# Optimization experiments

Measured on AMD Instinct MI355X. Metric: run time of the kernel, lower is better.

The kernel has to match this reference:

```python
import jax, jax.numpy as jnp
from jax import lax
import numpy as np

H, W = 4096, 4096
KH, KW = 15, 15


def setup_inputs() -> dict:
    key = jax.random.key(0)
    kx, kw = jax.random.split(key)
    X = jax.random.normal(kx, (H, W), dtype=jnp.float32)
    weight = jax.random.uniform(kw, (KH, KW), dtype=jnp.float32)
    bias = jnp.zeros((1,), dtype=jnp.float32)
    return {"X": X, "weight": weight, "bias": bias}


def reference(X, weight, bias):
    # Valid 2D cross-correlation (no kernel flip), matching corr2d.
    # lax.conv_general_dilated performs cross-correlation by default.
    out = lax.conv_general_dilated(
        X[None, None, :, :],            # NCHW: [1, 1, H, W]
        weight[None, None, :, :],       # OIHW: [1, 1, KH, KW]
        window_strides=(1, 1),
        padding="VALID",
    )
    return out[0, 0] + bias[0]          # [H-KH+1, W-KW+1]
```

## Files before the change

### kernel.cpp

```cpp
#include <hip/hip_runtime.h>
#include <hip/hip_bf16.h>

#define H_IN 4096
#define W_IN 4096
#define KH 15
#define KW 15
#define OH (H_IN - KH + 1)
#define OW (W_IN - KW + 1)

#define BM 64
#define BN 128
#define NJ (BN / 16)
#define SROWS (BM + KH - 1)
#define SCOLS 144
#define SSTR  152
#define SCH4 36
#define STAGE_N (SROWS * SCH4)
#define NLOAD 11

typedef __attribute__((ext_vector_type(8))) short short8;
typedef __attribute__((ext_vector_type(4))) float f32x4;

__device__ __forceinline__ ushort f2bf(float f) {
    __hip_bfloat16 h = __float2bfloat16(f);
    return __builtin_bit_cast(ushort, h);
}

__global__ __launch_bounds__(256)
void build_wfrags(const float* __restrict__ Wt, ushort* __restrict__ Bw)
{
    int idx = blockIdx.x * 256 + threadIdx.x;
    if (idx < KH * 64) {
        int kh = idx >> 6, l = idx & 63;
        int j = l & 15, k0 = (l >> 4) * 8;
        union { ushort u[8]; uint4 v; } t;
#pragma unroll
        for (int u = 0; u < 8; ++u) {
            int kw = k0 + u - j;
            t.u[u] = f2bf((kw >= 0 && kw < KW) ? Wt[kh * KW + kw] : 0.0f);
        }
        *reinterpret_cast<uint4*>(&Bw[idx * 8]) = t.v;
    }
}

__global__ __launch_bounds__(256, 4)
void conv2d_mfma_bf16(const float* __restrict__ X,
                      const ushort* __restrict__ Bw,
                      const float* __restrict__ Bias,
                      float* __restrict__ Out)
{
    __shared__ ushort s_x[SROWS * SSTR];

    const int tid = threadIdx.x;
    const int l = tid & 63;
    const int w = tid >> 6;
    const int ox0 = blockIdx.x * BN;
    const int oy0 = blockIdx.y * BM;
    const bool xint = (ox0 + SCOLS <= W_IN);

    float4 v[NLOAD];
#pragma unroll
    for (int k = 0; k < NLOAD; ++k) {
        int i = tid + 256 * k;
        if (i < STAGE_N) {
            int r  = i / SCH4;
            int c4 = i % SCH4;
            int gy = min(oy0 + r, H_IN - 1);
            const float* rp = X + (size_t)gy * W_IN;
            int gx = ox0 + c4 * 4;
            if (xint) {
                v[k] = *reinterpret_cast<const float4*>(rp + gx);
            } else {
                v[k].x = rp[min(gx + 0, W_IN - 1)];
                v[k].y = rp[min(gx + 1, W_IN - 1)];
                v[k].z = rp[min(gx + 2, W_IN - 1)];
                v[k].w = rp[min(gx + 3, W_IN - 1)];
            }
        }
    }
#pragma unroll
    for (int k = 0; k < NLOAD; ++k) {
        int i = tid + 256 * k;
        if (i < STAGE_N) {
            int r  = i / SCH4;
            int c4 = i % SCH4;
            uint2 pk;
            pk.x = (uint32_t)f2bf(v[k].x) | ((uint32_t)f2bf(v[k].y) << 16);
            pk.y = (uint32_t)f2bf(v[k].z) | ((uint32_t)f2bf(v[k].w) << 16);
            *reinterpret_cast<uint2*>(&s_x[r * SSTR + c4 * 4]) = pk;
        }
    }
    __syncthreads();

    const ushort* const bbase = Bw + l * 8;
    short8 bfr[KH];
#pragma unroll
    for (int kh = 0; kh < KH; ++kh)
        bfr[kh] = *reinterpret_cast<const short8*>(bbase + kh * 64 * 8);
    __builtin_amdgcn_sched_barrier(0);

    const ushort* const abase = &s_x[(w * 16 + (l & 15)) * SSTR + (l >> 4) * 8];

    f32x4 acc[NJ];
#pragma unroll
    for (int j = 0; j < NJ; ++j) acc[j] = (f32x4){0.f, 0.f, 0.f, 0.f};

#pragma unroll
    for (int kh = 0; kh < KH; ++kh) {
        const ushort* arow = abase + kh * SSTR;
#pragma unroll
        for (int j = 0; j < NJ; ++j) {
            short8 a = *reinterpret_cast<const short8*>(arow + j * 16);
            acc[j] = __builtin_amdgcn_mfma_f32_16x16x32_bf16(a, bfr[kh], acc[j], 0, 0, 0);
        }
    }

    const float b = Bias[0];
    const int orow0 = oy0 + w * 16 + (l >> 4) * 4;
    const int ocol  = ox0 + (l & 15);
    if (oy0 + BM <= OH && ox0 + BN <= OW) {
        float* op0 = &Out[(size_t)orow0 * OW + ocol];
#pragma unroll
        for (int j = 0; j < NJ; ++j) {
#pragma unroll
            for (int r = 0; r < 4; ++r)
                op0[(size_t)r * OW + j * 16] = acc[j][r] + b;
        }
    } else {
#pragma unroll
        for (int j = 0; j < NJ; ++j) {
            int oc = ocol + j * 16;
            if (oc < OW) {
#pragma unroll
                for (int r = 0; r < 4; ++r) {
                    int orow = orow0 + r;
                    if (orow < OH)
                        Out[(size_t)orow * OW + oc] = acc[j][r] + b;
                }
            }
        }
    }
}

extern "C" void kernel_launch(void* const* d_in, const int* in_sizes, int n_in,
                              void* d_out, int out_size, void* d_ws, size_t ws_size,
                              hipStream_t stream)
{
    const float* X    = (const float*)d_in[0];
    const float* Wt   = (const float*)d_in[1];
    const float* Bias = (const float*)d_in[2];
    float* Out        = (float*)d_out;
    ushort* Bw        = (ushort*)d_ws;

    hipLaunchKernelGGL(build_wfrags, dim3((KH * 64 + 255) / 256), dim3(256), 0, stream,
                       Wt, Bw);

    dim3 grid((OW + BN - 1) / BN,
              (OH + BM - 1) / BM);
    dim3 block(256);
    hipLaunchKernelGGL(conv2d_mfma_bf16, grid, block, 0, stream, X, Bw, Bias, Out);
}
```

Baseline: 43.62 us.

## Process two row tiles per block with register-prefetched next tile

Each block now handles two vertically adjacent output tiles. It issues the global loads for the next tile into registers before running the MFMA loop on the current one, then writes them to LDS between two barriers. Weight fragments are now loaded per kh inside the loop instead of being held in 15 registers up front, which lowers register pressure. The cost is half as many blocks, so less parallelism, plus extra barriers and weight reloads from global/L2 on every tile.

Result: slower. 48.44 us (+11.0%).

```diff
diff --git a/kernel.cpp b/kernel.cpp
--- a/kernel.cpp
+++ b/kernel.cpp
@@ -17,6 +17,7 @@
 #define SCH4 36
 #define STAGE_N (SROWS * SCH4)
 #define NLOAD 11
+#define TPB 2
 
 typedef __attribute__((ext_vector_type(8))) short short8;
 typedef __attribute__((ext_vector_type(4))) float f32x4;
@@ -43,22 +44,10 @@
     }
 }
 
-__global__ __launch_bounds__(256, 4)
-void conv2d_mfma_bf16(const float* __restrict__ X,
-                      const ushort* __restrict__ Bw,
-                      const float* __restrict__ Bias,
-                      float* __restrict__ Out)
+__device__ __forceinline__ void stage_issue(const float* __restrict__ X,
+                                            int oy0, int ox0, bool xint,
+                                            int tid, float4 (&v)[NLOAD])
 {
-    __shared__ ushort s_x[SROWS * SSTR];
-
-    const int tid = threadIdx.x;
-    const int l = tid & 63;
-    const int w = tid >> 6;
-    const int ox0 = blockIdx.x * BN;
-    const int oy0 = blockIdx.y * BM;
-    const bool xint = (ox0 + SCOLS <= W_IN);
-
-    float4 v[NLOAD];
 #pragma unroll
     for (int k = 0; k < NLOAD; ++k) {
         int i = tid + 256 * k;
@@ -78,6 +67,11 @@
             }
         }
     }
+}
+
+__device__ __forceinline__ void stage_write(ushort* __restrict__ s_x,
+                                            int tid, const float4 (&v)[NLOAD])
+{
 #pragma unroll
     for (int k = 0; k < NLOAD; ++k) {
         int i = tid + 256 * k;
@@ -90,54 +84,85 @@
             *reinterpret_cast<uint2*>(&s_x[r * SSTR + c4 * 4]) = pk;
         }
     }
+}
+
+__global__ __launch_bounds__(256, 4)
+void conv2d_mfma_pipe(const float* __restrict__ X,
+                      const ushort* __restrict__ Bw,
+                      const float* __restrict__ Bias,
+                      float* __restrict__ Out)
+{
+    __shared__ ushort s_x[SROWS * SSTR];
+
+    const int tid = threadIdx.x;
+    const int l = tid & 63;
+    const int w = tid >> 6;
+    const int ox0 = blockIdx.x * BN;
+    const int ty0 = blockIdx.y * TPB;
+    const bool xint = (ox0 + SCOLS <= W_IN);
+    const float b = Bias[0];
+
+    const ushort* const abase = &s_x[(w * 16 + (l & 15)) * SSTR + (l >> 4) * 8];
+    const ushort* const bbase = Bw + l * 8;
+
+    float4 v[NLOAD];
+
+    stage_issue(X, ty0 * BM, ox0, xint, tid, v);
+    stage_write(s_x, tid, v);
     __syncthreads();
 
-    const ushort* const bbase = Bw + l * 8;
-    short8 bfr[KH];
 #pragma unroll
-    for (int kh = 0; kh < KH; ++kh)
-        bfr[kh] = *reinterpret_cast<const short8*>(bbase + kh * 64 * 8);
-    __builtin_amdgcn_sched_barrier(0);
+    for (int t = 0; t < TPB; ++t) {
+        const int oy0 = (ty0 + t) * BM;
 
-    const ushort* const abase = &s_x[(w * 16 + (l & 15)) * SSTR + (l >> 4) * 8];
+        if (t + 1 < TPB)
+            stage_issue(X, (ty0 + t + 1) * BM, ox0, xint, tid, v);
+        __builtin_amdgcn_sched_barrier(0);
 
-    f32x4 acc[NJ];
+        f32x4 acc[NJ];
 #pragma unroll
-    for (int j = 0; j < NJ; ++j) acc[j] = (f32x4){0.f, 0.f, 0.f, 0.f};
+        for (int j = 0; j < NJ; ++j) acc[j] = (f32x4){0.f, 0.f, 0.f, 0.f};
 
 #pragma unroll
-    for (int kh = 0; kh < KH; ++kh) {
-        const ushort* arow = abase + kh * SSTR;
+        for (int kh = 0; kh < KH; ++kh) {
+            short8 bf = *reinterpret_cast<const short8*>(bbase + kh * 64 * 8);
+            const ushort* arow = abase + kh * SSTR;
 #pragma unroll
-        for (int j = 0; j < NJ; ++j) {
-            short8 a = *reinterpret_cast<const short8*>(arow + j * 16);
-            acc[j] = __builtin_amdgcn_mfma_f32_16x16x32_bf16(a, bfr[kh], acc[j], 0, 0, 0);
+            for (int j = 0; j < NJ; ++j) {
+                short8 a = *reinterpret_cast<const short8*>(arow + j * 16);
+                acc[j] = __builtin_amdgcn_mfma_f32_16x16x32_bf16(a, bf, acc[j], 0, 0, 0);
+            }
         }
-    }
 
-    const float b = Bias[0];
-    const int orow0 = oy0 + w * 16 + (l >> 4) * 4;
-    const int ocol  = ox0 + (l & 15);
-    if (oy0 + BM <= OH && ox0 + BN <= OW) {
-        float* op0 = &Out[(size_t)orow0 * OW + ocol];
+        const int orow0 = oy0 + w * 16 + (l >> 4) * 4;
+        const int ocol  = ox0 + (l & 15);
+        if (oy0 + BM <= OH && ox0 + BN <= OW) {
+            float* op0 = &Out[(size_t)orow0 * OW + ocol];
 #pragma unroll
-        for (int j = 0; j < NJ; ++j) {
+            for (int j = 0; j < NJ; ++j) {
 #pragma unroll
-            for (int r = 0; r < 4; ++r)
-                op0[(size_t)r * OW + j * 16] = acc[j][r] + b;
-        }
-    } else {
+                for (int r = 0; r < 4; ++r)
+                    op0[(size_t)r * OW + j * 16] = acc[j][r] + b;
+            }
+        } else {
 #pragma unroll
-        for (int j = 0; j < NJ; ++j) {
-            int oc = ocol + j * 16;
-            if (oc < OW) {
+            for (int j = 0; j < NJ; ++j) {
+                int oc = ocol + j * 16;
+                if (oc < OW) {
 #pragma unroll
-                for (int r = 0; r < 4; ++r) {
-                    int orow = orow0 + r;
-                    if (orow < OH)
-                        Out[(size_t)orow * OW + oc] = acc[j][r] + b;
+                    for (int r = 0; r < 4; ++r) {
+                        int orow = orow0 + r;
+                        if (orow < OH)
+                            Out[(size_t)orow * OW + oc] = acc[j][r] + b;
+                    }
                 }
             }
+        }
+
+        if (t + 1 < TPB) {
+            __syncthreads();
+            stage_write(s_x, tid, v);
+            __syncthreads();
         }
     }
 }
@@ -156,7 +181,7 @@
                        Wt, Bw);
 
     dim3 grid((OW + BN - 1) / BN,
-              (OH + BM - 1) / BM);
+              (OH + BM * TPB - 1) / (BM * TPB));
     dim3 block(256);
-    hipLaunchKernelGGL(conv2d_mfma_bf16, grid, block, 0, stream, X, Bw, Bias, Out);
+    hipLaunchKernelGGL(conv2d_mfma_pipe, grid, block, 0, stream, X, Bw, Bias, Out);
 }
```
